# Performance work log

Hardware: AMD Instinct MI355X
Metric: run time of the kernel (lower is better)

The kernel has to match this reference:

```python
import jax, jax.numpy as jnp
import numpy as np

TEMPERATURE = 0.07
EPS = 1e-8
B, D, C = 4096, 512, 10


def setup_inputs() -> dict:
    key = jax.random.key(0)
    k1, k2 = jax.random.split(key)
    features = jax.random.normal(k1, (B, D), dtype=jnp.float32)
    cls = jax.random.randint(k2, (B,), 0, C)
    labels = jax.nn.one_hot(cls, C, dtype=jnp.float32)  # [B, C] one-hot
    return {"features": features, "labels": labels}


def reference(features, labels):
    b = features.shape[0]
    # L2-normalize rows
    feats = features / jnp.linalg.norm(features, axis=1, keepdims=True)
    sim = jnp.clip(feats @ feats.T / TEMPERATURE, -20.0, 20.0)  # [B, B]
    eye = jnp.eye(b, dtype=bool)
    sim = jnp.where(eye, -jnp.inf, sim)  # mask self-similarity

    labels_norm = labels / (labels.sum(axis=1, keepdims=True) + EPS)
    label_sim = labels_norm @ labels_norm.T  # [B, B]
    label_sim = jnp.where(eye, 0.0, label_sim)
    pos_mask = label_sim > 0.1  # [B, B] bool

    exp_sim = jnp.exp(sim)  # diag -> exp(-inf) = 0
    pos_sum = jnp.sum(jnp.where(pos_mask, exp_sim, 0.0), axis=1)  # [B]
    all_sum = jnp.sum(exp_sim, axis=1)  # diag already zero => off-diagonal sum
    loss_i = -jnp.log(pos_sum / (all_sum + EPS) + EPS)  # [B]

    valid = jnp.any(pos_mask, axis=1)  # rows with >=1 positive
    n_valid = jnp.sum(valid.astype(jnp.float32))
    total = jnp.sum(jnp.where(valid, loss_i, 0.0))
    return jnp.where(n_valid > 0, total / n_valid, 0.0)
```

## Files before the change

### kernel.cpp

```cpp
#include <hip/hip_runtime.h>


#define B_ROWS 4096
#define D_DIM  512
#define C_CLS  10
#define NT     64
#define NTILES (NT * (NT + 1) / 2)
#define ASTRIDE 72

typedef __bf16 bf16x8 __attribute__((ext_vector_type(8)));
typedef float  f32x4  __attribute__((ext_vector_type(4)));

__global__ __launch_bounds__(256) void prep_kernel(
    const float* __restrict__ feats, const float* __restrict__ labels,
    __bf16* __restrict__ F, int* __restrict__ cls,
    float* __restrict__ pos_sum, float* __restrict__ all_sum) {
  const int w = threadIdx.x >> 6, lane = threadIdx.x & 63;
  const int row = blockIdx.x * 4 + w;
  const float* fr = feats + (size_t)row * D_DIM;
  float4 v0 = ((const float4*)fr)[2 * lane];
  float4 v1 = ((const float4*)fr)[2 * lane + 1];
  float ss = v0.x*v0.x + v0.y*v0.y + v0.z*v0.z + v0.w*v0.w
           + v1.x*v1.x + v1.y*v1.y + v1.z*v1.z + v1.w*v1.w;
  #pragma unroll
  for (int m = 1; m < 64; m <<= 1) ss += __shfl_xor(ss, m, 64);
  float inv = 1.0f / sqrtf(ss);

  bf16x8 o;
  o[0] = (__bf16)(v0.x * inv); o[1] = (__bf16)(v0.y * inv);
  o[2] = (__bf16)(v0.z * inv); o[3] = (__bf16)(v0.w * inv);
  o[4] = (__bf16)(v1.x * inv); o[5] = (__bf16)(v1.y * inv);
  o[6] = (__bf16)(v1.z * inv); o[7] = (__bf16)(v1.w * inv);
  *(bf16x8*)(F + (size_t)row * D_DIM + 8 * lane) = o;

  float lv = (lane < C_CLS) ? labels[(size_t)row * C_CLS + lane] : 0.f;
  unsigned long long m = __ballot(lv > 0.5f);
  if (lane == 0) {
    cls[row] = (int)(__ffsll((long long)m) - 1);
    pos_sum[row] = 0.f;
    all_sum[row] = 0.f;
  }
}

__global__ __launch_bounds__(256) void sim_kernel(
    const __bf16* __restrict__ F, const int* __restrict__ cls,
    float* __restrict__ pos_sum, float* __restrict__ all_sum) {
  __shared__ __align__(16) __bf16 Abuf[64][ASTRIDE];
  __shared__ __align__(16) __bf16 Bbuf[64][ASTRIDE];
  __shared__ int clsA[64], clsB[64];

  int rem = blockIdx.x, bi = 0, rowlen = NT;
  while (rem >= rowlen) { rem -= rowlen; ++bi; --rowlen; }
  const int bj = bi + rem;
  const int i0 = bi * 64, j0 = bj * 64;
  const bool offdiag = (bi != bj);

  const int t = threadIdx.x;
  const int w = t >> 6;
  const int lane = t & 63;
  const int q = lane >> 4;
  const int cl = lane & 15;

  if (t < 64)       clsA[t]      = cls[i0 + t];
  else if (t < 128) clsB[t - 64] = cls[j0 + t - 64];

  f32x4 acc[4];
  #pragma unroll
  for (int c = 0; c < 4; ++c) acc[c] = (f32x4){0.f, 0.f, 0.f, 0.f};

  const int sr = t >> 2;
  const int sc = (t & 3) * 16;

  for (int k0 = 0; k0 < D_DIM; k0 += 64) {
    __syncthreads();
    {
      const uint4* ga = (const uint4*)(F + (size_t)(i0 + sr) * D_DIM + k0 + sc);
      const uint4* gb = (const uint4*)(F + (size_t)(j0 + sr) * D_DIM + k0 + sc);
      uint4 a0 = ga[0], a1 = ga[1];
      uint4 b0 = gb[0], b1 = gb[1];
      *(uint4*)&Abuf[sr][sc]     = a0;
      *(uint4*)&Abuf[sr][sc + 8] = a1;
      *(uint4*)&Bbuf[sr][sc]     = b0;
      *(uint4*)&Bbuf[sr][sc + 8] = b1;
    }
    __syncthreads();

    #pragma unroll
    for (int kk = 0; kk < 64; kk += 32) {
      bf16x8 af = *(const bf16x8*)&Abuf[16*w + cl][kk + q*8];
      #pragma unroll
      for (int c = 0; c < 4; ++c) {
        bf16x8 bfr = *(const bf16x8*)&Bbuf[16*c + cl][kk + q*8];
        acc[c] = __builtin_amdgcn_mfma_f32_16x16x32_bf16(af, bfr, acc[c], 0, 0, 0);
      }
    }
  }

  const float invT = 1.0f / 0.07f;
  float sum_all[4] = {0.f, 0.f, 0.f, 0.f};
  float sum_pos[4] = {0.f, 0.f, 0.f, 0.f};
  float cs_all[4]  = {0.f, 0.f, 0.f, 0.f};
  float cs_pos[4]  = {0.f, 0.f, 0.f, 0.f};

  #pragma unroll
  for (int c = 0; c < 4; ++c) {
    const int jloc = 16*c + cl;
    const int gj = j0 + jloc;
    const int cj = clsB[jloc];
    #pragma unroll
    for (int r = 0; r < 4; ++r) {
      const int iloc = 16*w + q*4 + r;
      const int gi = i0 + iloc;
      float s = acc[c][r] * invT;
      s = fminf(fmaxf(s, -20.f), 20.f);
      const bool diag = (gi == gj);
      float e = diag ? 0.f : __expf(s);
      sum_all[r] += e;
      cs_all[c] += e;
      if (!diag && cj == clsA[iloc]) { sum_pos[r] += e; cs_pos[c] += e; }
    }
  }

  #pragma unroll
  for (int r = 0; r < 4; ++r) {
    float sa = sum_all[r], sp = sum_pos[r];
    #pragma unroll
    for (int m = 1; m < 16; m <<= 1) {
      sa += __shfl_xor(sa, m, 64);
      sp += __shfl_xor(sp, m, 64);
    }
    if (cl == 0) {
      const int gi = i0 + 16*w + q*4 + r;
      atomicAdd(&all_sum[gi], sa);
      atomicAdd(&pos_sum[gi], sp);
    }
  }

  if (offdiag) {
    #pragma unroll
    for (int c = 0; c < 4; ++c) {
      float sa = cs_all[c], sp = cs_pos[c];
      sa += __shfl_xor(sa, 16, 64); sa += __shfl_xor(sa, 32, 64);
      sp += __shfl_xor(sp, 16, 64); sp += __shfl_xor(sp, 32, 64);
      if (q == 0) {
        const int gj = j0 + 16*c + cl;
        atomicAdd(&all_sum[gj], sa);
        atomicAdd(&pos_sum[gj], sp);
      }
    }
  }
}

__global__ __launch_bounds__(256) void finalize_kernel(
    const float* __restrict__ pos_sum, const float* __restrict__ all_sum,
    float* __restrict__ out) {
  __shared__ float redT[4], redC[4];
  const int t = threadIdx.x;
  float total = 0.f, cnt = 0.f;
  for (int i = t; i < B_ROWS; i += 256) {
    float ps = pos_sum[i], as = all_sum[i];
    if (ps > 0.f) {
      total += -logf(ps / (as + 1e-8f) + 1e-8f);
      cnt += 1.f;
    }
  }
  #pragma unroll
  for (int m = 1; m < 64; m <<= 1) {
    total += __shfl_xor(total, m, 64);
    cnt   += __shfl_xor(cnt, m, 64);
  }
  if ((t & 63) == 0) { redT[t >> 6] = total; redC[t >> 6] = cnt; }
  __syncthreads();
  if (t == 0) {
    float T = 0.f, Cn = 0.f;
    #pragma unroll
    for (int i = 0; i < 4; ++i) { T += redT[i]; Cn += redC[i]; }
    out[0] = (Cn > 0.f) ? (T / Cn) : 0.f;
  }
}

extern "C" void kernel_launch(void* const* d_in, const int* in_sizes, int n_in,
                              void* d_out, int out_size, void* d_ws, size_t ws_size,
                              hipStream_t stream) {
  const float* features = (const float*)d_in[0];
  const float* labels   = (const float*)d_in[1];
  float* out = (float*)d_out;

  __bf16* F       = (__bf16*)d_ws;
  int*    cls     = (int*)((char*)d_ws + (size_t)B_ROWS * D_DIM * 2);
  float*  pos_sum = (float*)((char*)cls + B_ROWS * sizeof(int));
  float*  all_sum = pos_sum + B_ROWS;

  prep_kernel<<<B_ROWS / 4, 256, 0, stream>>>(features, labels, F, cls,
                                              pos_sum, all_sum);
  sim_kernel<<<NTILES, 256, 0, stream>>>(F, cls, pos_sum, all_sum);
  finalize_kernel<<<1, 256, 0, stream>>>(pos_sum, all_sum, out);
}
```

Before: 102.8 us.

## Load tiles directly to LDS with XOR swizzle and fuse finalize via ticket

Operand staging now uses global_load_lds, which writes directly into an unpadded LDS tile with an XOR-swizzled column layout to avoid bank conflicts. This removes the trip through registers and the padding. The separate finalize kernel is folded into sim_kernel: each block takes an atomic ticket after a threadfence, and the last block computes the final loss reduction. That saves one launch but adds a fence and an atomic to every block, and the result depends on correct memory ordering across blocks.

```diff
diff --git a/kernel.cpp b/kernel.cpp
--- a/kernel.cpp
+++ b/kernel.cpp
@@ -6,15 +6,21 @@
 #define C_CLS  10
 #define NT     64
 #define NTILES (NT * (NT + 1) / 2)
-#define ASTRIDE 72
 
 typedef __bf16 bf16x8 __attribute__((ext_vector_type(8)));
 typedef float  f32x4  __attribute__((ext_vector_type(4)));
+
+__device__ __forceinline__ void load_lds16(const __bf16* g, __bf16* l) {
+  __builtin_amdgcn_global_load_lds(
+      (const __attribute__((address_space(1))) unsigned int*)g,
+      (__attribute__((address_space(3))) unsigned int*)l, 16, 0, 0);
+}
 
 __global__ __launch_bounds__(256) void prep_kernel(
     const float* __restrict__ feats, const float* __restrict__ labels,
     __bf16* __restrict__ F, int* __restrict__ cls,
-    float* __restrict__ pos_sum, float* __restrict__ all_sum) {
+    float* __restrict__ pos_sum, float* __restrict__ all_sum,
+    int* __restrict__ done) {
   const int w = threadIdx.x >> 6, lane = threadIdx.x & 63;
   const int row = blockIdx.x * 4 + w;
   const float* fr = feats + (size_t)row * D_DIM;
@@ -40,14 +46,18 @@
     pos_sum[row] = 0.f;
     all_sum[row] = 0.f;
   }
+  if (blockIdx.x == 0 && threadIdx.x == 0) *done = 0;
 }
 
 __global__ __launch_bounds__(256) void sim_kernel(
     const __bf16* __restrict__ F, const int* __restrict__ cls,
-    float* __restrict__ pos_sum, float* __restrict__ all_sum) {
-  __shared__ __align__(16) __bf16 Abuf[64][ASTRIDE];
-  __shared__ __align__(16) __bf16 Bbuf[64][ASTRIDE];
+    float* __restrict__ pos_sum, float* __restrict__ all_sum,
+    int* __restrict__ done, float* __restrict__ out) {
+  __shared__ __align__(16) __bf16 Abuf[64 * 64];
+  __shared__ __align__(16) __bf16 Bbuf[64 * 64];
   __shared__ int clsA[64], clsB[64];
+  __shared__ int ticket_s;
+  __shared__ float redv[8];
 
   int rem = blockIdx.x, bi = 0, rowlen = NT;
   while (rem >= rowlen) { rem -= rowlen; ++bi; --rowlen; }
@@ -68,29 +78,29 @@
   #pragma unroll
   for (int c = 0; c < 4; ++c) acc[c] = (f32x4){0.f, 0.f, 0.f, 0.f};
 
-  const int sr = t >> 2;
-  const int sc = (t & 3) * 16;
+  const int srow = lane >> 3;
+  const int sg   = (lane & 7) ^ srow;
 
   for (int k0 = 0; k0 < D_DIM; k0 += 64) {
     __syncthreads();
-    {
-      const uint4* ga = (const uint4*)(F + (size_t)(i0 + sr) * D_DIM + k0 + sc);
-      const uint4* gb = (const uint4*)(F + (size_t)(j0 + sr) * D_DIM + k0 + sc);
-      uint4 a0 = ga[0], a1 = ga[1];
-      uint4 b0 = gb[0], b1 = gb[1];
-      *(uint4*)&Abuf[sr][sc]     = a0;
-      *(uint4*)&Abuf[sr][sc + 8] = a1;
-      *(uint4*)&Bbuf[sr][sc]     = b0;
-      *(uint4*)&Bbuf[sr][sc + 8] = b1;
+    #pragma unroll
+    for (int r = 0; r < 2; ++r) {
+      const int rowbase = w * 16 + r * 8;
+      load_lds16(F + (size_t)(i0 + rowbase + srow) * D_DIM + k0 + sg * 8,
+                 &Abuf[rowbase * 64]);
+      load_lds16(F + (size_t)(j0 + rowbase + srow) * D_DIM + k0 + sg * 8,
+                 &Bbuf[rowbase * 64]);
     }
     __syncthreads();
 
     #pragma unroll
     for (int kk = 0; kk < 64; kk += 32) {
-      bf16x8 af = *(const bf16x8*)&Abuf[16*w + cl][kk + q*8];
+      const int g = (kk >> 3) + q;
+      const int cc = g ^ (cl & 7);
+      bf16x8 af = *(const bf16x8*)&Abuf[(16 * w + cl) * 64 + cc * 8];
       #pragma unroll
       for (int c = 0; c < 4; ++c) {
-        bf16x8 bfr = *(const bf16x8*)&Bbuf[16*c + cl][kk + q*8];
+        bf16x8 bfr = *(const bf16x8*)&Bbuf[(16 * c + cl) * 64 + cc * 8];
         acc[c] = __builtin_amdgcn_mfma_f32_16x16x32_bf16(af, bfr, acc[c], 0, 0, 0);
       }
     }
@@ -149,33 +159,34 @@
       }
     }
   }
-}
-
-__global__ __launch_bounds__(256) void finalize_kernel(
-    const float* __restrict__ pos_sum, const float* __restrict__ all_sum,
-    float* __restrict__ out) {
-  __shared__ float redT[4], redC[4];
-  const int t = threadIdx.x;
-  float total = 0.f, cnt = 0.f;
-  for (int i = t; i < B_ROWS; i += 256) {
-    float ps = pos_sum[i], as = all_sum[i];
-    if (ps > 0.f) {
-      total += -logf(ps / (as + 1e-8f) + 1e-8f);
-      cnt += 1.f;
-    }
-  }
-  #pragma unroll
-  for (int m = 1; m < 64; m <<= 1) {
-    total += __shfl_xor(total, m, 64);
-    cnt   += __shfl_xor(cnt, m, 64);
-  }
-  if ((t & 63) == 0) { redT[t >> 6] = total; redC[t >> 6] = cnt; }
+
+  __threadfence();
   __syncthreads();
-  if (t == 0) {
-    float T = 0.f, Cn = 0.f;
-    #pragma unroll
-    for (int i = 0; i < 4; ++i) { T += redT[i]; Cn += redC[i]; }
-    out[0] = (Cn > 0.f) ? (T / Cn) : 0.f;
+  if (t == 0) ticket_s = atomicAdd(done, 1);
+  __syncthreads();
+  if (ticket_s == NTILES - 1) {
+    __threadfence();
+    float total = 0.f, cnt = 0.f;
+    for (int i = t; i < B_ROWS; i += 256) {
+      float ps = pos_sum[i], as = all_sum[i];
+      if (ps > 0.f) {
+        total += -__logf(ps / (as + 1e-8f) + 1e-8f);
+        cnt += 1.f;
+      }
+    }
+    #pragma unroll
+    for (int m = 1; m < 64; m <<= 1) {
+      total += __shfl_xor(total, m, 64);
+      cnt   += __shfl_xor(cnt, m, 64);
+    }
+    if ((t & 63) == 0) { redv[t >> 6] = total; redv[4 + (t >> 6)] = cnt; }
+    __syncthreads();
+    if (t == 0) {
+      float T = 0.f, Cn = 0.f;
+      #pragma unroll
+      for (int i = 0; i < 4; ++i) { T += redv[i]; Cn += redv[4 + i]; }
+      out[0] = (Cn > 0.f) ? (T / Cn) : 0.f;
+    }
   }
 }
 
@@ -190,9 +201,9 @@
   int*    cls     = (int*)((char*)d_ws + (size_t)B_ROWS * D_DIM * 2);
   float*  pos_sum = (float*)((char*)cls + B_ROWS * sizeof(int));
   float*  all_sum = pos_sum + B_ROWS;
+  int*    done    = (int*)(all_sum + B_ROWS);
 
   prep_kernel<<<B_ROWS / 4, 256, 0, stream>>>(features, labels, F, cls,
-                                              pos_sum, all_sum);
-  sim_kernel<<<NTILES, 256, 0, stream>>>(F, cls, pos_sum, all_sum);
-  finalize_kernel<<<1, 256, 0, stream>>>(pos_sum, all_sum, out);
-}
+                                              pos_sum, all_sum, done);
+  sim_kernel<<<NTILES, 256, 0, stream>>>(F, cls, pos_sum, all_sum, done, out);
+}
```

Result: slower. 220.2 us (+114.2%).
